# Optimization experiments

Hardware: AMD Instinct MI355X
Metric: run time of the kernel (lower is better)

Reference implementation:

```python
import jax, jax.numpy as jnp
import numpy as np

B = 65536
NODE, ENUM, ETYPE = 4, 6, 5
XDIM, EDIM, HDIM, ZDIM = 4, 5, 128, 32
ODIM = (2 * NODE + ETYPE) * ENUM  # 78
BETA = 0.005
EPS_SCALE = 0.01


def setup_inputs() -> dict:
    keys = jax.random.split(jax.random.key(0), 64)
    ki = iter(range(64))
    def rn(shape, s=1.0):
        return jax.random.normal(keys[next(ki)], shape, dtype=jnp.float32) * s
    # NAS-Bench-201 DAG edges per graph, batched as disjoint union
    base_src = jnp.array([0, 0, 1, 0, 1, 2], dtype=jnp.int32)
    base_dst = jnp.array([1, 2, 2, 3, 3, 3], dtype=jnp.int32)
    off = (jnp.arange(B, dtype=jnp.int32) * NODE)[:, None]
    edge_index = jnp.stack([(off + base_src).reshape(-1), (off + base_dst).reshape(-1)])
    s = 0.05
    inp = {
        'x': rn((B * NODE, XDIM)),
        'edge_attr': rn((B * ENUM, EDIM)),
        'arch_tensor': jax.random.uniform(keys[next(ki)], (B, ENUM, 2 * NODE + ETYPE), dtype=jnp.float32),
        'eps': rn((B, ZDIM)),
        'edge_index': edge_index,
        # conv0 (xdim=4 -> hdim=128)
        'c0_rw1': rn((XDIM, XDIM), s), 'c0_rb1': jnp.zeros((XDIM,), jnp.float32),
        'c0_rw2': rn((XDIM, HDIM), s), 'c0_rb2': jnp.zeros((HDIM,), jnp.float32),
        'c0_kw': rn((2 * XDIM + EDIM, HDIM), s),
        # conv1, conv2 (128 -> 128)
        'c1_rw1': rn((HDIM, HDIM), s), 'c1_rb1': jnp.zeros((HDIM,), jnp.float32),
        'c1_rw2': rn((HDIM, HDIM), s), 'c1_rb2': jnp.zeros((HDIM,), jnp.float32),
        'c1_kw': rn((2 * HDIM + EDIM, HDIM), s),
        'c2_rw1': rn((HDIM, HDIM), s), 'c2_rb1': jnp.zeros((HDIM,), jnp.float32),
        'c2_rw2': rn((HDIM, HDIM), s), 'c2_rb2': jnp.zeros((HDIM,), jnp.float32),
        'c2_kw': rn((2 * HDIM + EDIM, HDIM), s),
        # VAE heads
        'fc3_w': rn((HDIM, ZDIM), s), 'fc3_b': jnp.zeros((ZDIM,), jnp.float32),
        'fc4_w': rn((HDIM, ZDIM), s), 'fc4_b': jnp.zeros((ZDIM,), jnp.float32),
        'fc5_w': rn((ZDIM, HDIM), s), 'fc5_b': jnp.zeros((HDIM,), jnp.float32),
        # decoder: Resid_MLP(hdim,hdim) -> Resid_MLP(hdim,odim)
        'd1_mw': rn((HDIM, HDIM), s), 'd1_mb': jnp.zeros((HDIM,), jnp.float32),
        'd1_rw': rn((HDIM, HDIM), s), 'd1_rb': jnp.zeros((HDIM,), jnp.float32),
        'd2_mw': rn((HDIM, ODIM), s), 'd2_mb': jnp.zeros((ODIM,), jnp.float32),
        'd2_rw': rn((HDIM, ODIM), s), 'd2_rb': jnp.zeros((ODIM,), jnp.float32),
    }
    return inp


def _ce(logits, labels):
    # mean cross-entropy over batch*edges, like F.cross_entropy(..., reduction='mean')
    ls = jax.nn.log_softmax(logits, axis=-1)
    return -jnp.mean(jnp.take_along_axis(ls, labels[..., None], axis=-1))


def reference(x, edge_attr, arch_tensor, eps, edge_index,
              c0_rw1, c0_rb1, c0_rw2, c0_rb2, c0_kw,
              c1_rw1, c1_rb1, c1_rw2, c1_rb2, c1_kw,
              c2_rw1, c2_rb1, c2_rw2, c2_rb2, c2_kw,
              fc3_w, fc3_b, fc4_w, fc4_b, fc5_w, fc5_b,
              d1_mw, d1_mb, d1_rw, d1_rb, d2_mw, d2_mb, d2_rw, d2_rb):
    src, dst = edge_index[0], edge_index[1]
    n_nodes = x.shape[0]

    def conv(h, rw1, rb1, rw2, rb2, kw):
        resid = (h @ rw1 + rb1) @ rw2 + rb2  # residual_mlp: two Linears, no activation
        # message: leaky_relu(Linear(cat[x_i(target), x_j(source), edge_attr]))
        m = jax.nn.leaky_relu(jnp.concatenate([h[dst], h[src], edge_attr], axis=1) @ kw)
        return resid + jax.ops.segment_sum(m, dst, num_segments=n_nodes)  # aggr='add'

    h = conv(x, c0_rw1, c0_rb1, c0_rw2, c0_rb2, c0_kw)
    h = conv(h, c1_rw1, c1_rb1, c1_rw2, c1_rb2, c1_kw)
    h = conv(h, c2_rw1, c2_rb1, c2_rw2, c2_rb2, c2_kw)

    hg = h.reshape(B, NODE, HDIM).sum(axis=1)  # sum-pool nodes per graph
    mu = hg @ fc3_w + fc3_b
    logvar = hg @ fc4_w + fc4_b

    # reparameterize (training): z = (eps*eps_scale)*std + mu
    z = eps * EPS_SCALE * jnp.exp(0.5 * logvar) + mu

    # decode
    Hg = jnp.tanh(z @ fc5_w + fc5_b)
    h1 = jax.nn.leaky_relu(Hg @ d1_mw + d1_mb) + (Hg @ d1_rw + d1_rb)
    pred = jax.nn.leaky_relu(h1 @ d2_mw + d2_mb) + (h1 @ d2_rw + d2_rb)
    pred = pred.reshape(B, ENUM, 2 * NODE + ETYPE)
    in_pred, out_pred, et_pred = pred[:, :, :NODE], pred[:, :, NODE:2 * NODE], pred[:, :, 2 * NODE:]

    ti = jnp.argmax(arch_tensor[:, :, :NODE], axis=2)
    to = jnp.argmax(arch_tensor[:, :, NODE:2 * NODE], axis=2)
    te = jnp.argmax(arch_tensor[:, :, 2 * NODE:], axis=2)

    res = _ce(et_pred, te) + _ce(in_pred, ti) + _ce(out_pred, to)
    kld = -0.5 * jnp.mean(1.0 + logvar - mu ** 2 - jnp.exp(logvar))
    return res + BETA * kld
```

## Files before the change

kernel.cpp:

```cpp
#include <hip/hip_runtime.h>
#include <hip/hip_bf16.h>

#define BATCH 65536

typedef __bf16 bf16_t;
typedef __bf16 bf16x8 __attribute__((ext_vector_type(8)));
typedef float  f32x4  __attribute__((ext_vector_type(4)));

__device__ __forceinline__ f32x4 mfma16(bf16x8 a, bf16x8 b, f32x4 c) {
    return __builtin_amdgcn_mfma_f32_16x16x32_bf16(a, b, c, 0, 0, 0);
}
__device__ __forceinline__ int swz128(int row, int col) {
    return row * 128 + ((((col >> 3) ^ (row & 7)) << 3) | (col & 7));
}

struct PrepSrcs { const float* p[16]; };

__global__ __launch_bounds__(256) void prep_weights(PrepSrcs ps,
    const float* __restrict__ c0_rb1, const float* __restrict__ c0_rb2,
    const float* __restrict__ c1_rb1, const float* __restrict__ c1_rb2,
    const float* __restrict__ c2_rb1, const float* __restrict__ c2_rb2,
    bf16_t* __restrict__ dst, float* __restrict__ bias)
{
    int f = blockIdx.x;
    if (f >= 344) {
        int c = threadIdx.x;
        if (c < 128) {
            if (f == 344) {
                const float* rw2 = ps.p[11];
                float s = c1_rb2[c];
                for (int m = 0; m < 128; m++) s += c1_rb1[m] * rw2[m * 128 + c];
                bias[c] = s;
            } else if (f == 345) {
                const float* rw2 = ps.p[13];
                float s = c2_rb2[c];
                for (int m = 0; m < 128; m++) s += c2_rb1[m] * rw2[m * 128 + c];
                bias[128 + c] = s;
            } else {
                const float* rw2 = ps.p[15];
                float s = c0_rb2[c];
                for (int m = 0; m < 4; m++) s += c0_rb1[m] * rw2[m * 128 + c];
                bias[256 + c] = s;
            }
        }
        return;
    }
    const int BASE[17] = {0,32,64,96,128,160,192,200,208,216,248,280,300,320,328,336,344};
    const int SRC[16]  = {10,0,0,12,1,1,2,3,4,5,6,7,8,14,9,9};
    const int KTt[16]  = {4,4,4,4,4,4,4,4,1,4,4,4,4,1,1,1};
    const int KLIM[16] = {128,128,128,128,128,128,128,128,32,128,128,128,128,4,4,4};
    const int NLIM[16] = {128,128,128,128,128,128,32,32,128,128,128,78,78,128,128,128};
    const int STR[16]  = {128,128,128,128,128,128,32,32,128,128,128,78,78,128,128,128};
    const int RO[16]   = {0,0,128,0,0,128,0,0,0,0,0,0,0,0,0,4};

    int ei = 0;
    while (ei < 15 && BASE[ei + 1] <= f) ei++;
    int lf = f - BASE[ei];
    int kt = lf % KTt[ei];
    int nt = lf / KTt[ei];
    #pragma unroll
    for (int r2 = 0; r2 < 2; r2++) {
        int idx = threadIdx.x * 2 + r2;
        int l = idx >> 3, j = idx & 7;
        int row = 32 * kt + 8 * (l >> 4) + j;
        int col = 16 * nt + (l & 15);
        float v = 0.f;
        if (ei == 0 || ei == 3) {
            const float* rw1 = ps.p[ei == 0 ? 10 : 12];
            const float* rw2 = ps.p[ei == 0 ? 11 : 13];
            for (int m = 0; m < 128; m++) v += rw1[row * 128 + m] * rw2[m * 128 + col];
        } else if (ei == 13) {
            if (row < 4) {
                const float* rw1 = ps.p[14];
                const float* rw2 = ps.p[15];
                for (int m = 0; m < 4; m++) v += rw1[row * 4 + m] * rw2[m * 128 + col];
            }
        } else {
            if (row < KLIM[ei] && col < NLIM[ei])
                v = ps.p[SRC[ei]][(row + RO[ei]) * STR[ei] + col];
        }
        dst[f * 512 + idx] = (bf16_t)v;
    }
}

__device__ __forceinline__ void edge_update(float o[4], const f32x4& kd, const f32x4& ks,
                                            const float* pe, const float* kwe)
{
    float mm;
    mm = kd[1] + ks[0] + (pe[0]*kwe[0]+pe[1]*kwe[1]+pe[2]*kwe[2]+pe[3]*kwe[3]+pe[4]*kwe[4]);
    mm = fmaxf(mm, 0.01f * mm); o[1] += mm;
    mm = kd[2] + ks[0] + (pe[5]*kwe[0]+pe[6]*kwe[1]+pe[7]*kwe[2]+pe[8]*kwe[3]+pe[9]*kwe[4]);
    mm = fmaxf(mm, 0.01f * mm); o[2] += mm;
    mm = kd[2] + ks[1] + (pe[10]*kwe[0]+pe[11]*kwe[1]+pe[12]*kwe[2]+pe[13]*kwe[3]+pe[14]*kwe[4]);
    mm = fmaxf(mm, 0.01f * mm); o[2] += mm;
    mm = kd[3] + ks[0] + (pe[15]*kwe[0]+pe[16]*kwe[1]+pe[17]*kwe[2]+pe[18]*kwe[3]+pe[19]*kwe[4]);
    mm = fmaxf(mm, 0.01f * mm); o[3] += mm;
    mm = kd[3] + ks[1] + (pe[20]*kwe[0]+pe[21]*kwe[1]+pe[22]*kwe[2]+pe[23]*kwe[3]+pe[24]*kwe[4]);
    mm = fmaxf(mm, 0.01f * mm); o[3] += mm;
    mm = kd[3] + ks[2] + (pe[25]*kwe[0]+pe[26]*kwe[1]+pe[27]*kwe[2]+pe[28]*kwe[3]+pe[29]*kwe[4]);
    mm = fmaxf(mm, 0.01f * mm); o[3] += mm;
}

template<bool LAST>
__device__ __forceinline__ void conv_pass(
    bf16_t* lA, const float* lea, const bf16_t* wf,
    const float* kwe_base, const float* b12,
    int w, int q, int lr, int lane)
{
    bf16x8 ah[2][4];
    #pragma unroll
    for (int mt = 0; mt < 2; mt++) {
        int row = 32 * w + 16 * mt + lr;
        #pragma unroll
        for (int kt = 0; kt < 4; kt++)
            ah[mt][kt] = *(const bf16x8*)(lA + row * 128 + (((4 * kt + q) ^ (row & 7)) << 3));
    }
    __syncthreads();

    const bf16_t* wfd = wf + 32 * 512;
    const bf16_t* wfs = wf + 64 * 512;
    #pragma unroll 1
    for (int nt = 0; nt < 8; nt++) {
        int col = 16 * nt + lr;
        float bv = b12[col];
        f32x4 rr[2], kd[2], ks[2];
        rr[0] = (f32x4){bv, bv, bv, bv}; rr[1] = rr[0];
        kd[0] = (f32x4){0.f, 0.f, 0.f, 0.f}; kd[1] = kd[0];
        ks[0] = kd[0]; ks[1] = kd[0];
        #pragma unroll
        for (int kt = 0; kt < 4; kt++) {
            bf16x8 bw = *(const bf16x8*)(wf  + (nt * 4 + kt) * 512 + lane * 8);
            bf16x8 bd = *(const bf16x8*)(wfd + (nt * 4 + kt) * 512 + lane * 8);
            bf16x8 bs = *(const bf16x8*)(wfs + (nt * 4 + kt) * 512 + lane * 8);
            #pragma unroll
            for (int mt = 0; mt < 2; mt++) {
                rr[mt] = mfma16(ah[mt][kt], bw, rr[mt]);
                kd[mt] = mfma16(ah[mt][kt], bd, kd[mt]);
                ks[mt] = mfma16(ah[mt][kt], bs, ks[mt]);
            }
        }
        float kwe[5];
        #pragma unroll
        for (int i = 0; i < 5; i++) kwe[i] = kwe_base[i * 128 + col];
        #pragma unroll
        for (int mt = 0; mt < 2; mt++) {
            int el = 8 * w + 4 * mt + q;
            const float* pe = lea + el * 30;
            float o[4] = {rr[mt][0], rr[mt][1], rr[mt][2], rr[mt][3]};
            edge_update(o, kd[mt], ks[mt], pe, kwe);
            if (!LAST) {
                #pragma unroll
                for (int j = 0; j < 4; j++)
                    lA[swz128(32 * w + 16 * mt + 4 * q + j, col)] = (bf16_t)o[j];
            } else {
                lA[swz128(el, col)] = (bf16_t)(o[0] + o[1] + o[2] + o[3]);
            }
        }
    }
    __syncthreads();
}

__device__ __forceinline__ float ce_group(const float* p, const float* a, int off, int len) {
    float m = p[off];
    #pragma unroll
    for (int i = 1; i < 5; i++) if (i < len) m = fmaxf(m, p[off + i]);
    float am = a[off]; int lbl = 0;
    #pragma unroll
    for (int i = 1; i < 5; i++) if (i < len) { float av = a[off + i]; if (av > am) { am = av; lbl = i; } }
    float s = 0.f;
    #pragma unroll
    for (int i = 0; i < 5; i++) if (i < len) s += __expf(p[off + i] - m);
    return (m + __logf(s)) - p[off + lbl];
}

__global__ __launch_bounds__(256, 3) void fused_kernel(
    const float* __restrict__ x, const float* __restrict__ ea,
    const float* __restrict__ arch, const float* __restrict__ eps,
    const bf16_t* __restrict__ wfr, const float* __restrict__ bias,
    const float* __restrict__ c0_kw, const float* __restrict__ c1_kw,
    const float* __restrict__ c2_kw,
    const float* __restrict__ fc3_b, const float* __restrict__ fc4_b,
    const float* __restrict__ fc5_b, const float* __restrict__ d1_mb,
    const float* __restrict__ d1_rb, const float* __restrict__ d2_mb,
    const float* __restrict__ d2_rb,
    float* __restrict__ ce_part, float* __restrict__ kld_part)
{
    __shared__ __align__(16) bf16_t lA[128 * 128];
    __shared__ __align__(16) float  lsc[960];

    const int tid = threadIdx.x;
    const int w = tid >> 6, lane = tid & 63, q = lane >> 4, lr = lane & 15;
    const int e0 = blockIdx.x * 32;
    const int r0 = e0 * 4;
    const float* lea = lsc;

    if (tid < 240) ((float4*)lsc)[tid] = ((const float4*)(ea + (size_t)e0 * 30))[tid];
    __syncthreads();

    {
        bf16x8 ax[2];
        #pragma unroll
        for (int mt = 0; mt < 2; mt++) {
            float4 xv = {0.f, 0.f, 0.f, 0.f};
            if (q == 0) xv = *(const float4*)(x + (size_t)(r0 + 32 * w + 16 * mt + lr) * 4);
            bf16x8 a = {0, 0, 0, 0, 0, 0, 0, 0};
            a[0] = (bf16_t)xv.x; a[1] = (bf16_t)xv.y; a[2] = (bf16_t)xv.z; a[3] = (bf16_t)xv.w;
            ax[mt] = a;
        }
        const bf16_t* w0f = wfr + 320 * 512;
        const bf16_t* wdf = wfr + 328 * 512;
        const bf16_t* wsf = wfr + 336 * 512;
        const float* b0 = bias + 256;
        const float* kwe_base = c0_kw + 8 * 128;
        #pragma unroll 1
        for (int nt = 0; nt < 8; nt++) {
            int col = 16 * nt + lr;
            float bb = b0[col];
            f32x4 rr[2], kd[2], ks[2];
            rr[0] = (f32x4){bb, bb, bb, bb}; rr[1] = rr[0];
            kd[0] = (f32x4){0.f, 0.f, 0.f, 0.f}; kd[1] = kd[0];
            ks[0] = kd[0]; ks[1] = kd[0];
            bf16x8 bw0 = *(const bf16x8*)(w0f + nt * 512 + lane * 8);
            bf16x8 bwa = *(const bf16x8*)(wdf + nt * 512 + lane * 8);
            bf16x8 bwb = *(const bf16x8*)(wsf + nt * 512 + lane * 8);
            #pragma unroll
            for (int mt = 0; mt < 2; mt++) {
                rr[mt] = mfma16(ax[mt], bw0, rr[mt]);
                kd[mt] = mfma16(ax[mt], bwa, kd[mt]);
                ks[mt] = mfma16(ax[mt], bwb, ks[mt]);
            }
            float kwe[5];
            #pragma unroll
            for (int i = 0; i < 5; i++) kwe[i] = kwe_base[i * 128 + col];
            #pragma unroll
            for (int mt = 0; mt < 2; mt++) {
                int el = 8 * w + 4 * mt + q;
                const float* pe = lea + el * 30;
                float o[4] = {rr[mt][0], rr[mt][1], rr[mt][2], rr[mt][3]};
                edge_update(o, kd[mt], ks[mt], pe, kwe);
                #pragma unroll
                for (int j = 0; j < 4; j++)
                    lA[swz128(32 * w + 16 * mt + 4 * q + j, col)] = (bf16_t)o[j];
            }
        }
    }
    __syncthreads();

    conv_pass<false>(lA, lea, wfr,            c1_kw + 256 * 128, bias,       w, q, lr, lane);
    conv_pass<true >(lA, lea, wfr + 96 * 512, c2_kw + 256 * 128, bias + 128, w, q, lr, lane);

    const int mtd = w >> 1, tp = w & 1;
    const int grow = 16 * mtd + lr;

    bf16x8 ag[4];
    #pragma unroll
    for (int kt = 0; kt < 4; kt++)
        ag[kt] = *(const bf16x8*)(lA + grow * 128 + (((4 * kt + q) ^ (grow & 7)) << 3));
    float bmu = fc3_b[16 * tp + lr], blv = fc4_b[16 * tp + lr];
    f32x4 amu = (f32x4){bmu, bmu, bmu, bmu}, alv = (f32x4){blv, blv, blv, blv};
    const bf16_t* f3 = wfr + (192 + tp * 4) * 512;
    const bf16_t* f4 = wfr + (200 + tp * 4) * 512;
    #pragma unroll
    for (int kt = 0; kt < 4; kt++) {
        amu = mfma16(ag[kt], *(const bf16x8*)(f3 + kt * 512 + lane * 8), amu);
        alv = mfma16(ag[kt], *(const bf16x8*)(f4 + kt * 512 + lane * 8), alv);
    }
    float kldp = 0.f;
    bf16_t* lz = lA + 4096;
    #pragma unroll
    for (int j = 0; j < 4; j++) {
        int el = 16 * mtd + 4 * q + j;
        float mu = amu[j], lv = alv[j];
        kldp += 1.f + lv - mu * mu - __expf(lv);
        int c = 16 * tp + lr;
        float zz = eps[(size_t)(e0 + el) * 32 + c] * 0.01f * __expf(0.5f * lv) + mu;
        lz[el * 32 + ((((c >> 3) ^ (el & 3)) << 3) | (c & 7))] = (bf16_t)zz;
    }
    __syncthreads();

    bf16_t* lHg = lA + 6144;
    bf16x8 az = *(const bf16x8*)(lz + grow * 32 + ((q ^ (grow & 3)) << 3));
    const bf16_t* f5 = wfr + 208 * 512;
    #pragma unroll 1
    for (int i = 0; i < 4; i++) {
        int nt = 4 * tp + i;
        float b = fc5_b[16 * nt + lr];
        f32x4 a = (f32x4){b, b, b, b};
        a = mfma16(az, *(const bf16x8*)(f5 + nt * 512 + lane * 8), a);
        #pragma unroll
        for (int j = 0; j < 4; j++) {
            float ex2 = __expf(2.f * a[j]);
            float th = 1.f - 2.f / (ex2 + 1.f);
            lHg[swz128(16 * mtd + 4 * q + j, 16 * nt + lr)] = (bf16_t)th;
        }
    }
    __syncthreads();

    bf16x8 aHg[4];
    #pragma unroll
    for (int kt = 0; kt < 4; kt++)
        aHg[kt] = *(const bf16x8*)(lHg + grow * 128 + (((4 * kt + q) ^ (grow & 7)) << 3));
    const bf16_t* wd1m = wfr + 216 * 512;
    const bf16_t* wd1r = wfr + 248 * 512;
    #pragma unroll 1
    for (int i = 0; i < 4; i++) {
        int nt = 4 * tp + i;
        int col = 16 * nt + lr;
        float bm = d1_mb[col], br = d1_rb[col];
        f32x4 am = (f32x4){bm, bm, bm, bm}, ar = (f32x4){br, br, br, br};
        #pragma unroll
        for (int kt = 0; kt < 4; kt++) {
            am = mfma16(aHg[kt], *(const bf16x8*)(wd1m + (nt * 4 + kt) * 512 + lane * 8), am);
            ar = mfma16(aHg[kt], *(const bf16x8*)(wd1r + (nt * 4 + kt) * 512 + lane * 8), ar);
        }
        #pragma unroll
        for (int j = 0; j < 4; j++) {
            float v = fmaxf(am[j], 0.01f * am[j]) + ar[j];
            lA[swz128(16 * mtd + 4 * q + j, col)] = (bf16_t)v;
        }
    }
    __syncthreads();

    bf16x8 a1[4];
    #pragma unroll
    for (int kt = 0; kt < 4; kt++)
        a1[kt] = *(const bf16x8*)(lA + grow * 128 + (((4 * kt + q) ^ (grow & 7)) << 3));
    float* lpred = (float*)(lA + 10240);
    const bf16_t* wd2m = wfr + 280 * 512;
    const bf16_t* wd2r = wfr + 300 * 512;
    const int ntbeg = tp ? 3 : 0, ntend = tp ? 5 : 3;
    #pragma unroll 1
    for (int nt = ntbeg; nt < ntend; nt++) {
        int col = 16 * nt + lr;
        float bm = (col < 78) ? d2_mb[col] : 0.f;
        float br = (col < 78) ? d2_rb[col] : 0.f;
        f32x4 pm = (f32x4){bm, bm, bm, bm}, pr = (f32x4){br, br, br, br};
        #pragma unroll
        for (int kt = 0; kt < 4; kt++) {
            pm = mfma16(a1[kt], *(const bf16x8*)(wd2m + (nt * 4 + kt) * 512 + lane * 8), pm);
            pr = mfma16(a1[kt], *(const bf16x8*)(wd2r + (nt * 4 + kt) * 512 + lane * 8), pr);
        }
        #pragma unroll
        for (int j = 0; j < 4; j++) {
            float v = fmaxf(pm[j], 0.01f * pm[j]) + pr[j];
            lpred[(16 * mtd + 4 * q + j) * 80 + col] = v;
        }
    }
    __syncthreads();

    float ces = 0.f;
    if (tid < 192) {
        int el = tid / 6, u = tid - el * 6;
        const float* pa = arch + ((size_t)(e0 + el) * 6 + u) * 13;
        const float* pp = lpred + el * 80 + u * 13;
        ces  = ce_group(pp, pa, 0, 4);
        ces += ce_group(pp, pa, 4, 4);
        ces += ce_group(pp, pa, 8, 5);
    }
    __syncthreads();
    float* lred = lsc;
    lred[tid] = ces;
    __syncthreads();
    for (int s = 128; s > 0; s >>= 1) {
        if (tid < s) lred[tid] += lred[tid + s];
        __syncthreads();
    }
    if (tid == 0) ce_part[blockIdx.x] = lred[0];
    __syncthreads();
    lred[tid] = kldp;
    __syncthreads();
    for (int s = 128; s > 0; s >>= 1) {
        if (tid < s) lred[tid] += lred[tid + s];
        __syncthreads();
    }
    if (tid == 0) kld_part[blockIdx.x] = lred[0];
}

__global__ __launch_bounds__(256) void final_reduce(
    const float* __restrict__ ce_part, const float* __restrict__ kld_part,
    float* __restrict__ out)
{
    __shared__ float r[256];
    int tid = threadIdx.x;
    float c = 0.f, k = 0.f;
    for (int i = tid; i < 2048; i += 256) { c += ce_part[i]; k += kld_part[i]; }
    r[tid] = c; __syncthreads();
    for (int s = 128; s > 0; s >>= 1) { if (tid < s) r[tid] += r[tid + s]; __syncthreads(); }
    float ctot = r[0];
    __syncthreads();
    r[tid] = k; __syncthreads();
    for (int s = 128; s > 0; s >>= 1) { if (tid < s) r[tid] += r[tid + s]; __syncthreads(); }
    if (tid == 0) {
        float ktot = r[0];
        out[0] = ctot / (65536.f * 6.f) - 0.5f * 0.005f * (ktot / (65536.f * 32.f));
    }
}

extern "C" void kernel_launch(void* const* d_in, const int* in_sizes, int n_in,
                              void* d_out, int out_size, void* d_ws, size_t ws_size,
                              hipStream_t stream)
{
    const float* x      = (const float*)d_in[0];
    const float* ea     = (const float*)d_in[1];
    const float* arch   = (const float*)d_in[2];
    const float* eps    = (const float*)d_in[3];
    const float* c0_rw1 = (const float*)d_in[5];
    const float* c0_rb1 = (const float*)d_in[6];
    const float* c0_rw2 = (const float*)d_in[7];
    const float* c0_rb2 = (const float*)d_in[8];
    const float* c0_kw  = (const float*)d_in[9];
    const float* c1_rw1 = (const float*)d_in[10];
    const float* c1_rb1 = (const float*)d_in[11];
    const float* c1_rw2 = (const float*)d_in[12];
    const float* c1_rb2 = (const float*)d_in[13];
    const float* c1_kw  = (const float*)d_in[14];
    const float* c2_rw1 = (const float*)d_in[15];
    const float* c2_rb1 = (const float*)d_in[16];
    const float* c2_rw2 = (const float*)d_in[17];
    const float* c2_rb2 = (const float*)d_in[18];
    const float* c2_kw  = (const float*)d_in[19];
    const float* fc3_w  = (const float*)d_in[20];
    const float* fc3_b  = (const float*)d_in[21];
    const float* fc4_w  = (const float*)d_in[22];
    const float* fc4_b  = (const float*)d_in[23];
    const float* fc5_w  = (const float*)d_in[24];
    const float* fc5_b  = (const float*)d_in[25];
    const float* d1_mw  = (const float*)d_in[26];
    const float* d1_mb  = (const float*)d_in[27];
    const float* d1_rw  = (const float*)d_in[28];
    const float* d1_rb  = (const float*)d_in[29];
    const float* d2_mw  = (const float*)d_in[30];
    const float* d2_mb  = (const float*)d_in[31];
    const float* d2_rw  = (const float*)d_in[32];
    const float* d2_rb  = (const float*)d_in[33];

    bf16_t* wfr      = (bf16_t*)d_ws;
    float*  bias     = (float*)((char*)d_ws + 352256);
    float*  ce_part  = (float*)((char*)d_ws + 353792);
    float*  kld_part = (float*)((char*)d_ws + 361984);

    PrepSrcs ps;
    ps.p[0] = c1_kw;  ps.p[1] = c2_kw;  ps.p[2] = fc3_w;  ps.p[3] = fc4_w;
    ps.p[4] = fc5_w;  ps.p[5] = d1_mw;  ps.p[6] = d1_rw;  ps.p[7] = d2_mw;
    ps.p[8] = d2_rw;  ps.p[9] = c0_kw;  ps.p[10] = c1_rw1; ps.p[11] = c1_rw2;
    ps.p[12] = c2_rw1; ps.p[13] = c2_rw2; ps.p[14] = c0_rw1; ps.p[15] = c0_rw2;

    prep_weights<<<347, 256, 0, stream>>>(ps, c0_rb1, c0_rb2, c1_rb1, c1_rb2,
                                          c2_rb1, c2_rb2, wfr, bias);
    fused_kernel<<<BATCH / 32, 256, 0, stream>>>(
        x, ea, arch, eps, wfr, bias, c0_kw, c1_kw, c2_kw,
        fc3_b, fc4_b, fc5_b, d1_mb, d1_rb, d2_mb, d2_rb,
        ce_part, kld_part);
    final_reduce<<<1, 256, 0, stream>>>(ce_part, kld_part, (float*)d_out);
}
```

Baseline: 143.0 us.

## Compute edge-attribute projections with MFMA instead of scalar FMA loops

Moves the per-edge edge_attr·kw 5-term dot products, once done with scalar FMAs from LDS-staged edge attributes, onto MFMA. Each conv pass now runs a small bf16 matmul per output tile, writes it to a shared scratch buffer, and reads it back in the edge update. Edge weight slices are packed into new prep_weights fragments, and the edge-attribute LDS staging and global kw reads are removed. In exchange there are extra MFMA issues, scratch LDS traffic and bf16 rounding of the edge terms.

New measurement: 129.7 us. -9.3%, faster.

```diff
diff --git a/kernel.cpp b/kernel.cpp
--- a/kernel.cpp
+++ b/kernel.cpp
@@ -23,15 +23,15 @@
     bf16_t* __restrict__ dst, float* __restrict__ bias)
 {
     int f = blockIdx.x;
-    if (f >= 344) {
+    if (f >= 368) {
         int c = threadIdx.x;
         if (c < 128) {
-            if (f == 344) {
+            if (f == 368) {
                 const float* rw2 = ps.p[11];
                 float s = c1_rb2[c];
                 for (int m = 0; m < 128; m++) s += c1_rb1[m] * rw2[m * 128 + c];
                 bias[c] = s;
-            } else if (f == 345) {
+            } else if (f == 369) {
                 const float* rw2 = ps.p[13];
                 float s = c2_rb2[c];
                 for (int m = 0; m < 128; m++) s += c2_rb1[m] * rw2[m * 128 + c];
@@ -45,16 +45,16 @@
         }
         return;
     }
-    const int BASE[17] = {0,32,64,96,128,160,192,200,208,216,248,280,300,320,328,336,344};
-    const int SRC[16]  = {10,0,0,12,1,1,2,3,4,5,6,7,8,14,9,9};
-    const int KTt[16]  = {4,4,4,4,4,4,4,4,1,4,4,4,4,1,1,1};
-    const int KLIM[16] = {128,128,128,128,128,128,128,128,32,128,128,128,128,4,4,4};
-    const int NLIM[16] = {128,128,128,128,128,128,32,32,128,128,128,78,78,128,128,128};
-    const int STR[16]  = {128,128,128,128,128,128,32,32,128,128,128,78,78,128,128,128};
-    const int RO[16]   = {0,0,128,0,0,128,0,0,0,0,0,0,0,0,0,4};
+    const int BASE[20] = {0,32,64,96,128,160,192,200,208,216,248,280,300,320,328,336,344,352,360,368};
+    const int SRC[19]  = {10,0,0,12,1,1,2,3,4,5,6,7,8,14,9,9,9,0,1};
+    const int KTt[19]  = {4,4,4,4,4,4,4,4,1,4,4,4,4,1,1,1,1,1,1};
+    const int KLIM[19] = {128,128,128,128,128,128,128,128,32,128,128,128,128,4,4,4,5,5,5};
+    const int NLIM[19] = {128,128,128,128,128,128,32,32,128,128,128,78,78,128,128,128,128,128,128};
+    const int STR[19]  = {128,128,128,128,128,128,32,32,128,128,128,78,78,128,128,128,128,128,128};
+    const int RO[19]   = {0,0,128,0,0,128,0,0,0,0,0,0,0,0,0,4,8,256,256};
 
     int ei = 0;
-    while (ei < 15 && BASE[ei + 1] <= f) ei++;
+    while (ei < 18 && BASE[ei + 1] <= f) ei++;
     int lf = f - BASE[ei];
     int kt = lf % KTt[ei];
     int nt = lf / KTt[ei];
@@ -84,27 +84,36 @@
 }
 
 __device__ __forceinline__ void edge_update(float o[4], const f32x4& kd, const f32x4& ks,
-                                            const float* pe, const float* kwe)
+                                            const float* et)
 {
     float mm;
-    mm = kd[1] + ks[0] + (pe[0]*kwe[0]+pe[1]*kwe[1]+pe[2]*kwe[2]+pe[3]*kwe[3]+pe[4]*kwe[4]);
-    mm = fmaxf(mm, 0.01f * mm); o[1] += mm;
-    mm = kd[2] + ks[0] + (pe[5]*kwe[0]+pe[6]*kwe[1]+pe[7]*kwe[2]+pe[8]*kwe[3]+pe[9]*kwe[4]);
-    mm = fmaxf(mm, 0.01f * mm); o[2] += mm;
-    mm = kd[2] + ks[1] + (pe[10]*kwe[0]+pe[11]*kwe[1]+pe[12]*kwe[2]+pe[13]*kwe[3]+pe[14]*kwe[4]);
-    mm = fmaxf(mm, 0.01f * mm); o[2] += mm;
-    mm = kd[3] + ks[0] + (pe[15]*kwe[0]+pe[16]*kwe[1]+pe[17]*kwe[2]+pe[18]*kwe[3]+pe[19]*kwe[4]);
-    mm = fmaxf(mm, 0.01f * mm); o[3] += mm;
-    mm = kd[3] + ks[1] + (pe[20]*kwe[0]+pe[21]*kwe[1]+pe[22]*kwe[2]+pe[23]*kwe[3]+pe[24]*kwe[4]);
-    mm = fmaxf(mm, 0.01f * mm); o[3] += mm;
-    mm = kd[3] + ks[2] + (pe[25]*kwe[0]+pe[26]*kwe[1]+pe[27]*kwe[2]+pe[28]*kwe[3]+pe[29]*kwe[4]);
-    mm = fmaxf(mm, 0.01f * mm); o[3] += mm;
+    mm = kd[1] + ks[0] + et[0]; mm = fmaxf(mm, 0.01f * mm); o[1] += mm;
+    mm = kd[2] + ks[0] + et[1]; mm = fmaxf(mm, 0.01f * mm); o[2] += mm;
+    mm = kd[2] + ks[1] + et[2]; mm = fmaxf(mm, 0.01f * mm); o[2] += mm;
+    mm = kd[3] + ks[0] + et[3]; mm = fmaxf(mm, 0.01f * mm); o[3] += mm;
+    mm = kd[3] + ks[1] + et[4]; mm = fmaxf(mm, 0.01f * mm); o[3] += mm;
+    mm = kd[3] + ks[2] + et[5]; mm = fmaxf(mm, 0.01f * mm); o[3] += mm;
+}
+
+__device__ __forceinline__ void compute_et(bf16_t* etb, const bf16x8* aet,
+                                           const bf16_t* wet, int nt,
+                                           int w, int q, int lr, int lane)
+{
+    bf16x8 be = *(const bf16x8*)(wet + nt * 512 + lane * 8);
+    #pragma unroll
+    for (int t = 0; t < 3; t++) {
+        f32x4 z = {0.f, 0.f, 0.f, 0.f};
+        z = mfma16(aet[t], be, z);
+        #pragma unroll
+        for (int j = 0; j < 4; j++)
+            etb[(48 * w + 16 * t + 4 * q + j) * 20 + lr] = (bf16_t)z[j];
+    }
 }
 
 template<bool LAST>
 __device__ __forceinline__ void conv_pass(
-    bf16_t* lA, const float* lea, const bf16_t* wf,
-    const float* kwe_base, const float* b12,
+    bf16_t* lA, bf16_t* etb, const bf16x8* aet,
+    const bf16_t* wf, const bf16_t* wet, const float* b12,
     int w, int q, int lr, int lane)
 {
     bf16x8 ah[2][4];
@@ -122,6 +131,7 @@
     #pragma unroll 1
     for (int nt = 0; nt < 8; nt++) {
         int col = 16 * nt + lr;
+        compute_et(etb, aet, wet, nt, w, q, lr, lane);
         float bv = b12[col];
         f32x4 rr[2], kd[2], ks[2];
         rr[0] = (f32x4){bv, bv, bv, bv}; rr[1] = rr[0];
@@ -139,15 +149,15 @@
                 ks[mt] = mfma16(ah[mt][kt], bs, ks[mt]);
             }
         }
-        float kwe[5];
-        #pragma unroll
-        for (int i = 0; i < 5; i++) kwe[i] = kwe_base[i * 128 + col];
         #pragma unroll
         for (int mt = 0; mt < 2; mt++) {
             int el = 8 * w + 4 * mt + q;
-            const float* pe = lea + el * 30;
+            float et6[6];
+            #pragma unroll
+            for (int u = 0; u < 6; u++)
+                et6[u] = (float)etb[(48 * w + 24 * mt + 6 * q + u) * 20 + lr];
             float o[4] = {rr[mt][0], rr[mt][1], rr[mt][2], rr[mt][3]};
-            edge_update(o, kd[mt], ks[mt], pe, kwe);
+            edge_update(o, kd[mt], ks[mt], et6);
             if (!LAST) {
                 #pragma unroll
                 for (int j = 0; j < 4; j++)
@@ -177,8 +187,6 @@
     const float* __restrict__ x, const float* __restrict__ ea,
     const float* __restrict__ arch, const float* __restrict__ eps,
     const bf16_t* __restrict__ wfr, const float* __restrict__ bias,
-    const float* __restrict__ c0_kw, const float* __restrict__ c1_kw,
-    const float* __restrict__ c2_kw,
     const float* __restrict__ fc3_b, const float* __restrict__ fc4_b,
     const float* __restrict__ fc5_b, const float* __restrict__ d1_mb,
     const float* __restrict__ d1_rb, const float* __restrict__ d2_mb,
@@ -186,16 +194,25 @@
     float* __restrict__ ce_part, float* __restrict__ kld_part)
 {
     __shared__ __align__(16) bf16_t lA[128 * 128];
-    __shared__ __align__(16) float  lsc[960];
+    __shared__ __align__(16) bf16_t etb[192 * 20];
 
     const int tid = threadIdx.x;
     const int w = tid >> 6, lane = tid & 63, q = lane >> 4, lr = lane & 15;
     const int e0 = blockIdx.x * 32;
     const int r0 = e0 * 4;
-    const float* lea = lsc;
-
-    if (tid < 240) ((float4*)lsc)[tid] = ((const float4*)(ea + (size_t)e0 * 30))[tid];
-    __syncthreads();
+
+    bf16x8 aet[3];
+    #pragma unroll
+    for (int t = 0; t < 3; t++) {
+        bf16x8 a = {0, 0, 0, 0, 0, 0, 0, 0};
+        if (q == 0) {
+            int e = 48 * w + 16 * t + lr;
+            const float* pe = ea + ((size_t)e0 * 6 + e) * 5;
+            #pragma unroll
+            for (int i = 0; i < 5; i++) a[i] = (bf16_t)pe[i];
+        }
+        aet[t] = a;
+    }
 
     {
         bf16x8 ax[2];
@@ -210,11 +227,12 @@
         const bf16_t* w0f = wfr + 320 * 512;
         const bf16_t* wdf = wfr + 328 * 512;
         const bf16_t* wsf = wfr + 336 * 512;
+        const bf16_t* wef = wfr + 344 * 512;
         const float* b0 = bias + 256;
-        const float* kwe_base = c0_kw + 8 * 128;
         #pragma unroll 1
         for (int nt = 0; nt < 8; nt++) {
             int col = 16 * nt + lr;
+            compute_et(etb, aet, wef, nt, w, q, lr, lane);
             float bb = b0[col];
             f32x4 rr[2], kd[2], ks[2];
             rr[0] = (f32x4){bb, bb, bb, bb}; rr[1] = rr[0];
@@ -229,15 +247,14 @@
                 kd[mt] = mfma16(ax[mt], bwa, kd[mt]);
                 ks[mt] = mfma16(ax[mt], bwb, ks[mt]);
             }
-            float kwe[5];
-            #pragma unroll
-            for (int i = 0; i < 5; i++) kwe[i] = kwe_base[i * 128 + col];
             #pragma unroll
             for (int mt = 0; mt < 2; mt++) {
-                int el = 8 * w + 4 * mt + q;
-                const float* pe = lea + el * 30;
+                float et6[6];
+                #pragma unroll
+                for (int u = 0; u < 6; u++)
+                    et6[u] = (float)etb[(48 * w + 24 * mt + 6 * q + u) * 20 + lr];
                 float o[4] = {rr[mt][0], rr[mt][1], rr[mt][2], rr[mt][3]};
-                edge_update(o, kd[mt], ks[mt], pe, kwe);
+                edge_update(o, kd[mt], ks[mt], et6);
                 #pragma unroll
                 for (int j = 0; j < 4; j++)
                     lA[swz128(32 * w + 16 * mt + 4 * q + j, col)] = (bf16_t)o[j];
@@ -246,8 +263,8 @@
     }
     __syncthreads();
 
-    conv_pass<false>(lA, lea, wfr,            c1_kw + 256 * 128, bias,       w, q, lr, lane);
-    conv_pass<true >(lA, lea, wfr + 96 * 512, c2_kw + 256 * 128, bias + 128, w, q, lr, lane);
+    conv_pass<false>(lA, etb, aet, wfr,            wfr + 352 * 512, bias,       w, q, lr, lane);
+    conv_pass<true >(lA, etb, aet, wfr + 96 * 512, wfr + 360 * 512, bias + 128, w, q, lr, lane);
 
     const int mtd = w >> 1, tp = w & 1;
     const int grow = 16 * mtd + lr;
@@ -358,7 +375,7 @@
         ces += ce_group(pp, pa, 8, 5);
     }
     __syncthreads();
-    float* lred = lsc;
+    float* lred = (float*)etb;
     lred[tid] = ces;
     __syncthreads();
     for (int s = 128; s > 0; s >>= 1) {
@@ -435,9 +452,9 @@
     const float* d2_rb  = (const float*)d_in[33];
 
     bf16_t* wfr      = (bf16_t*)d_ws;
-    float*  bias     = (float*)((char*)d_ws + 352256);
-    float*  ce_part  = (float*)((char*)d_ws + 353792);
-    float*  kld_part = (float*)((char*)d_ws + 361984);
+    float*  bias     = (float*)((char*)d_ws + 376832);
+    float*  ce_part  = (float*)((char*)d_ws + 378368);
+    float*  kld_part = (float*)((char*)d_ws + 386560);
 
     PrepSrcs ps;
     ps.p[0] = c1_kw;  ps.p[1] = c2_kw;  ps.p[2] = fc3_w;  ps.p[3] = fc4_w;
@@ -445,10 +462,10 @@
     ps.p[8] = d2_rw;  ps.p[9] = c0_kw;  ps.p[10] = c1_rw1; ps.p[11] = c1_rw2;
     ps.p[12] = c2_rw1; ps.p[13] = c2_rw2; ps.p[14] = c0_rw1; ps.p[15] = c0_rw2;
 
-    prep_weights<<<347, 256, 0, stream>>>(ps, c0_rb1, c0_rb2, c1_rb1, c1_rb2,
+    prep_weights<<<371, 256, 0, stream>>>(ps, c0_rb1, c0_rb2, c1_rb1, c1_rb2,
                                           c2_rb1, c2_rb2, wfr, bias);
     fused_kernel<<<BATCH / 32, 256, 0, stream>>>(
-        x, ea, arch, eps, wfr, bias, c0_kw, c1_kw, c2_kw,
+        x, ea, arch, eps, wfr, bias,
         fc3_b, fc4_b, fc5_b, d1_mb, d1_rb, d2_mb, d2_rb,
         ce_part, kld_part);
     final_reduce<<<1, 256, 0, stream>>>(ce_part, kld_part, (float*)d_out);
```
